# Performance work log

Hardware: AMD Instinct MI355X
Metric: run time of the kernel (lower is better)

## Reference

```python
import jax, jax.numpy as jnp
import numpy as np

NUM_USERS = 200000
NUM_ITEMS = 100000
N_NODES = NUM_USERS + NUM_ITEMS
NNZ = 4000000
LATENT_DIM = 64
N_LAYERS = 3


def setup_inputs() -> dict:
    key = jax.random.key(0)
    k1, k2, k3, k4, k5 = jax.random.split(key, 5)
    user_emb = jax.random.normal(k1, (NUM_USERS, LATENT_DIM), dtype=jnp.float32) * 0.1
    item_emb = jax.random.normal(k2, (NUM_ITEMS, LATENT_DIM), dtype=jnp.float32) * 0.1
    vals = jax.random.uniform(k3, (NNZ,), dtype=jnp.float32)
    rows = jax.random.randint(k4, (NNZ,), 0, N_NODES)
    cols = jax.random.randint(k5, (NNZ,), 0, N_NODES)
    return {"user_emb": user_emb, "item_emb": item_emb, "vals": vals,
            "rows": rows, "cols": cols}


def _spmm(vals, rows, cols, x):
    # y[r] += vals[e] * x[cols[e]]  -- COO SpMM, equivalent to torch.sparse.mm
    msgs = vals[:, None] * x[cols]          # [nnz, d]
    return jax.ops.segment_sum(msgs, rows, num_segments=N_NODES)


def reference(user_emb, item_emb, vals, rows, cols):
    # LightGCN.computer(), eval path: L = ones, no dropout, norm_emb=False
    all_emb = jnp.concatenate([user_emb, item_emb], axis=0)  # [N, d]
    emb = all_emb
    acc = all_emb
    for _ in range(N_LAYERS):
        emb = _spmm(vals, rows, cols, emb)
        acc = acc + emb
    light_out = acc / jnp.asarray(N_LAYERS + 1, dtype=acc.dtype)  # mean over layers
    users = light_out[:NUM_USERS]
    items = light_out[NUM_USERS:]
    return users, items
```

## Files before the change

kernel.cpp:

```cpp
#include <hip/hip_runtime.h>

#define NUM_USERS 200000
#define NUM_ITEMS 100000
#define N_NODES   300000
#define NNZ       4000000
#define DIM       64
#define N_ELEM   ((size_t)N_NODES * DIM)

static __device__ __forceinline__ float bf2f(unsigned short v) {
    return __uint_as_float(((unsigned int)v) << 16);
}
static __device__ __forceinline__ unsigned short f2bf(float f) {
    unsigned int u = __float_as_uint(f);
    u = (u + 0x7FFF + ((u >> 16) & 1)) >> 16;
    return (unsigned short)u;
}

__global__ void lgcn_hist(const int4* __restrict__ rows4, int* __restrict__ cnt) {
    int i = blockIdx.x * blockDim.x + threadIdx.x;
    if (i >= NNZ / 4) return;
    int4 r = rows4[i];
    atomicAdd(&cnt[r.x], 1);
    atomicAdd(&cnt[r.y], 1);
    atomicAdd(&cnt[r.z], 1);
    atomicAdd(&cnt[r.w], 1);
}

__global__ void lgcn_alloc(const int* __restrict__ cnt, int2* __restrict__ desc,
                           int* __restrict__ fill, int* __restrict__ cursor) {
    int r = blockIdx.x * blockDim.x + threadIdx.x;
    int lane = threadIdx.x & 63;
    int c = (r < N_NODES) ? cnt[r] : 0;
    int s = c;
    #pragma unroll
    for (int o = 1; o < 64; o <<= 1) {
        int t = __shfl_up(s, o);
        if (lane >= o) s += t;
    }
    int total = __shfl(s, 63);
    int wbase = 0;
    if (lane == 63) wbase = atomicAdd(cursor, total);
    wbase = __shfl(wbase, 63);
    if (r < N_NODES) {
        int b = wbase + (s - c);
        desc[r] = make_int2(b, c);
        fill[r] = b;
    }
}

__global__ void lgcn_scatter(const int* __restrict__ rows, const int* __restrict__ cols,
                             const float* __restrict__ vals, int* __restrict__ fill,
                             int2* __restrict__ sc) {
    int e = blockIdx.x * blockDim.x + threadIdx.x;
    if (e >= NNZ) return;
    int r = rows[e];
    int p = atomicAdd(&fill[r], 1);
    sc[p] = make_int2(cols[e], __float_as_int(vals[e]));
}

template<int MODE>
__global__ __launch_bounds__(256) void lgcn_spmm_csr(
    const int2* __restrict__ desc, const int2* __restrict__ sc,
    const float* __restrict__ user_emb, const float* __restrict__ item_emb,
    const unsigned short* __restrict__ cur, unsigned short* __restrict__ nxt,
    float* __restrict__ out)
{
    int row  = blockIdx.x * 4 + (threadIdx.x >> 6);
    int lane = threadIdx.x & 63;
    if (row >= N_NODES) return;
    int2 d = desc[row];
    int b = d.x, n = d.y;
    float acc0 = 0.f, acc1 = 0.f, acc2 = 0.f, acc3 = 0.f;

    for (int k0 = 0; k0 < n; k0 += 64) {
        int m = min(64, n - k0);
        int c = 0, vbits = 0;
        if (lane < m) {
            int2 cv = sc[b + k0 + lane];
            c = cv.x; vbits = cv.y;
        }
        int m8 = (m + 7) & ~7;
        for (int j = 0; j < m8; j += 8) {
            int   cc[8];
            float vv[8];
            #pragma unroll
            for (int t = 0; t < 8; ++t) {
                cc[t] = __shfl(c, j + t);
                vv[t] = __int_as_float(__shfl(vbits, j + t));
            }
            float x[8];
            #pragma unroll
            for (int t = 0; t < 8; ++t) {
                if constexpr (MODE == 0) {
                    x[t] = (cc[t] < NUM_USERS)
                         ? user_emb[(size_t)cc[t] * DIM + lane]
                         : item_emb[(size_t)(cc[t] - NUM_USERS) * DIM + lane];
                } else {
                    x[t] = bf2f(cur[(size_t)cc[t] * DIM + lane]);
                }
            }
            acc0 += vv[0] * x[0];
            acc1 += vv[1] * x[1];
            acc2 += vv[2] * x[2];
            acc3 += vv[3] * x[3];
            acc0 += vv[4] * x[4];
            acc1 += vv[5] * x[5];
            acc2 += vv[6] * x[6];
            acc3 += vv[7] * x[7];
        }
    }

    float acc = (acc0 + acc1) + (acc2 + acc3);
    size_t o = (size_t)row * DIM + lane;
    if constexpr (MODE == 0) {
        float own = (row < NUM_USERS)
                  ? user_emb[o]
                  : item_emb[(size_t)(row - NUM_USERS) * DIM + lane];
        nxt[o] = f2bf(acc);
        out[o] = 0.25f * (own + acc);
    } else if constexpr (MODE == 1) {
        nxt[o] = f2bf(acc);
        out[o] += 0.25f * acc;
    } else {
        out[o] += 0.25f * acc;
    }
}

extern "C" void kernel_launch(void* const* d_in, const int* in_sizes, int n_in,
                              void* d_out, int out_size, void* d_ws, size_t ws_size,
                              hipStream_t stream) {
    const float* user_emb = (const float*)d_in[0];
    const float* item_emb = (const float*)d_in[1];
    const float* vals     = (const float*)d_in[2];
    const int*   rows     = (const int*)d_in[3];
    const int*   cols     = (const int*)d_in[4];
    float* out = (float*)d_out;

    char* ws = (char*)d_ws;
    size_t off = 0;
    unsigned short* buf0 = (unsigned short*)(ws + off); off += N_ELEM * 2;
    unsigned short* buf1 = (unsigned short*)(ws + off); off += N_ELEM * 2;
    int2*  sc       = (int2*)(ws + off); off += (size_t)NNZ * 8;
    int*   row_cnt  = (int*) (ws + off); off += (size_t)N_NODES * 4;
    int*   cursor   = (int*) (ws + off); off += 256;
    int2*  row_desc = (int2*)(ws + off); off += (size_t)N_NODES * 8;
    int*   row_fill = (int*) (ws + off); off += (size_t)N_NODES * 4;

    const int BLK = 256;
    dim3 grid_edge((NNZ + BLK - 1) / BLK);
    dim3 grid_edge4((NNZ / 4 + BLK - 1) / BLK);
    dim3 grid_node((N_NODES + BLK - 1) / BLK);
    dim3 grid_spmm((N_NODES + 3) / 4);

    hipMemsetAsync(row_cnt, 0, (size_t)N_NODES * 4 + 256, stream);
    lgcn_hist<<<grid_edge4, BLK, 0, stream>>>((const int4*)rows, row_cnt);
    lgcn_alloc<<<grid_node, BLK, 0, stream>>>(row_cnt, row_desc, row_fill, cursor);
    lgcn_scatter<<<grid_edge, BLK, 0, stream>>>(rows, cols, vals, row_fill, sc);

    lgcn_spmm_csr<0><<<grid_spmm, BLK, 0, stream>>>(
        row_desc, sc, user_emb, item_emb, nullptr, buf0, out);
    lgcn_spmm_csr<1><<<grid_spmm, BLK, 0, stream>>>(
        row_desc, sc, nullptr, nullptr, buf0, buf1, out);
    lgcn_spmm_csr<2><<<grid_spmm, BLK, 0, stream>>>(
        row_desc, sc, nullptr, nullptr, buf1, nullptr, out);
}
```

Measured before the change: 952.5 us.

## Build CSR via two-level bucket sort and gather bf16 inputs in all layers

```diff
diff --git a/kernel.cpp b/kernel.cpp
--- a/kernel.cpp
+++ b/kernel.cpp
@@ -7,6 +7,10 @@
 #define DIM       64
 #define N_ELEM   ((size_t)N_NODES * DIM)
 
+#define BKT_SHIFT 6
+#define NBKT      ((N_NODES + 63) >> 6)
+#define PAD       32
+
 static __device__ __forceinline__ float bf2f(unsigned short v) {
     return __uint_as_float(((unsigned int)v) << 16);
 }
@@ -16,21 +20,33 @@
     return (unsigned short)u;
 }
 
-__global__ void lgcn_hist(const int4* __restrict__ rows4, int* __restrict__ cnt) {
+__global__ void lgcn_convert(const float4* __restrict__ user4,
+                             const float4* __restrict__ item4,
+                             ushort4* __restrict__ bufC) {
+    size_t i = (size_t)blockIdx.x * blockDim.x + threadIdx.x;
+    const size_t n4 = N_ELEM / 4, nu4 = (size_t)NUM_USERS * DIM / 4;
+    if (i >= n4) return;
+    float4 v = (i < nu4) ? user4[i] : item4[i - nu4];
+    ushort4 o;
+    o.x = f2bf(v.x); o.y = f2bf(v.y); o.z = f2bf(v.z); o.w = f2bf(v.w);
+    bufC[i] = o;
+}
+
+__global__ void lgcn_bhist(const int4* __restrict__ rows4, int* __restrict__ bcnt) {
     int i = blockIdx.x * blockDim.x + threadIdx.x;
     if (i >= NNZ / 4) return;
     int4 r = rows4[i];
-    atomicAdd(&cnt[r.x], 1);
-    atomicAdd(&cnt[r.y], 1);
-    atomicAdd(&cnt[r.z], 1);
-    atomicAdd(&cnt[r.w], 1);
-}
-
-__global__ void lgcn_alloc(const int* __restrict__ cnt, int2* __restrict__ desc,
-                           int* __restrict__ fill, int* __restrict__ cursor) {
-    int r = blockIdx.x * blockDim.x + threadIdx.x;
+    atomicAdd(&bcnt[(r.x >> BKT_SHIFT) * PAD], 1);
+    atomicAdd(&bcnt[(r.y >> BKT_SHIFT) * PAD], 1);
+    atomicAdd(&bcnt[(r.z >> BKT_SHIFT) * PAD], 1);
+    atomicAdd(&bcnt[(r.w >> BKT_SHIFT) * PAD], 1);
+}
+
+__global__ void lgcn_balloc(const int* __restrict__ bcnt, int* __restrict__ bbase,
+                            int* __restrict__ bfill, int* __restrict__ cursor) {
+    int b = blockIdx.x * blockDim.x + threadIdx.x;
     int lane = threadIdx.x & 63;
-    int c = (r < N_NODES) ? cnt[r] : 0;
+    int c = (b < NBKT) ? bcnt[b * PAD] : 0;
     int s = c;
     #pragma unroll
     for (int o = 1; o < 64; o <<= 1) {
@@ -41,28 +57,69 @@
     int wbase = 0;
     if (lane == 63) wbase = atomicAdd(cursor, total);
     wbase = __shfl(wbase, 63);
-    if (r < N_NODES) {
-        int b = wbase + (s - c);
-        desc[r] = make_int2(b, c);
-        fill[r] = b;
-    }
-}
-
-__global__ void lgcn_scatter(const int* __restrict__ rows, const int* __restrict__ cols,
-                             const float* __restrict__ vals, int* __restrict__ fill,
-                             int2* __restrict__ sc) {
+    if (b < NBKT) {
+        int base = wbase + (s - c);
+        bbase[b] = base;
+        bfill[b * PAD] = base;
+    }
+}
+
+__global__ void lgcn_append(const int* __restrict__ rows, const int* __restrict__ cols,
+                            const float* __restrict__ vals, int* __restrict__ bfill,
+                            int2* __restrict__ staging) {
     int e = blockIdx.x * blockDim.x + threadIdx.x;
     if (e >= NNZ) return;
     int r = rows[e];
-    int p = atomicAdd(&fill[r], 1);
-    sc[p] = make_int2(cols[e], __float_as_int(vals[e]));
+    int b = r >> BKT_SHIFT;
+    int p = atomicAdd(&bfill[b * PAD], 1);
+    staging[p] = make_int2(((r & 63) << 19) | cols[e], __float_as_int(vals[e]));
+}
+
+__global__ __launch_bounds__(256) void lgcn_bsort(
+    const int2* __restrict__ staging, const int* __restrict__ bbase,
+    const int* __restrict__ bcnt, int2* __restrict__ desc, int2* __restrict__ sc)
+{
+    __shared__ int cnt64[64], fill64[64];
+    int b   = blockIdx.x;
+    int tid = threadIdx.x;
+    if (tid < 64) cnt64[tid] = 0;
+    __syncthreads();
+    int base = bbase[b];
+    int n    = bcnt[b * PAD];
+
+    for (int i = tid; i < n; i += 256)
+        atomicAdd(&cnt64[staging[base + i].x >> 19], 1);
+    __syncthreads();
+
+    if (tid < 64) {
+        int c = cnt64[tid];
+        int s = c;
+        #pragma unroll
+        for (int o = 1; o < 64; o <<= 1) {
+            int t = __shfl_up(s, o);
+            if (tid >= o) s += t;
+        }
+        int off = s - c;
+        fill64[tid] = off;
+        int row = (b << BKT_SHIFT) + tid;
+        if (row < N_NODES) desc[row] = make_int2(base + off, c);
+    }
+    __syncthreads();
+
+    for (int i = tid; i < n; i += 256) {
+        int2 e = staging[base + i];
+        int lr = e.x >> 19;
+        int p = atomicAdd(&fill64[lr], 1);
+        sc[base + p] = make_int2(e.x & 0x7FFFF, e.y);
+    }
 }
 
 template<int MODE>
 __global__ __launch_bounds__(256) void lgcn_spmm_csr(
     const int2* __restrict__ desc, const int2* __restrict__ sc,
+    const unsigned short* __restrict__ cur, unsigned short* __restrict__ nxt,
     const float* __restrict__ user_emb, const float* __restrict__ item_emb,
-    const unsigned short* __restrict__ cur, unsigned short* __restrict__ nxt,
+    const unsigned short* __restrict__ e1buf, const unsigned short* __restrict__ e2buf,
     float* __restrict__ out)
 {
     int row  = blockIdx.x * 4 + (threadIdx.x >> 6);
@@ -90,15 +147,8 @@
             }
             float x[8];
             #pragma unroll
-            for (int t = 0; t < 8; ++t) {
-                if constexpr (MODE == 0) {
-                    x[t] = (cc[t] < NUM_USERS)
-                         ? user_emb[(size_t)cc[t] * DIM + lane]
-                         : item_emb[(size_t)(cc[t] - NUM_USERS) * DIM + lane];
-                } else {
-                    x[t] = bf2f(cur[(size_t)cc[t] * DIM + lane]);
-                }
-            }
+            for (int t = 0; t < 8; ++t)
+                x[t] = bf2f(cur[(size_t)cc[t] * DIM + lane]);
             acc0 += vv[0] * x[0];
             acc1 += vv[1] * x[1];
             acc2 += vv[2] * x[2];
@@ -112,17 +162,13 @@
 
     float acc = (acc0 + acc1) + (acc2 + acc3);
     size_t o = (size_t)row * DIM + lane;
-    if constexpr (MODE == 0) {
+    if constexpr (MODE == 1) {
+        nxt[o] = f2bf(acc);
+    } else {
         float own = (row < NUM_USERS)
                   ? user_emb[o]
                   : item_emb[(size_t)(row - NUM_USERS) * DIM + lane];
-        nxt[o] = f2bf(acc);
-        out[o] = 0.25f * (own + acc);
-    } else if constexpr (MODE == 1) {
-        nxt[o] = f2bf(acc);
-        out[o] += 0.25f * acc;
-    } else {
-        out[o] += 0.25f * acc;
+        out[o] = 0.25f * (own + bf2f(e1buf[o]) + bf2f(e2buf[o]) + acc);
     }
 }
 
@@ -138,29 +184,37 @@
 
     char* ws = (char*)d_ws;
     size_t off = 0;
+    unsigned short* bufC = (unsigned short*)(ws + off); off += N_ELEM * 2;
     unsigned short* buf0 = (unsigned short*)(ws + off); off += N_ELEM * 2;
     unsigned short* buf1 = (unsigned short*)(ws + off); off += N_ELEM * 2;
-    int2*  sc       = (int2*)(ws + off); off += (size_t)NNZ * 8;
-    int*   row_cnt  = (int*) (ws + off); off += (size_t)N_NODES * 4;
-    int*   cursor   = (int*) (ws + off); off += 256;
-    int2*  row_desc = (int2*)(ws + off); off += (size_t)N_NODES * 8;
-    int*   row_fill = (int*) (ws + off); off += (size_t)N_NODES * 4;
+    int2* staging = (int2*)(ws + off); off += (size_t)NNZ * 8;
+    int2* sc      = (int2*)(ws + off); off += (size_t)NNZ * 8;
+    int2* desc    = (int2*)(ws + off); off += (size_t)N_NODES * 8;
+    int*  bcnt    = (int*) (ws + off); off += (size_t)NBKT * PAD * 4;
+    int*  cursor  = (int*) (ws + off); off += 256;
+    int*  bbase   = (int*) (ws + off); off += (size_t)NBKT * 4;
+    int*  bfill   = (int*) (ws + off); off += (size_t)NBKT * PAD * 4;
 
     const int BLK = 256;
+    dim3 grid_conv((unsigned)((N_ELEM / 4 + BLK - 1) / BLK));
     dim3 grid_edge((NNZ + BLK - 1) / BLK);
     dim3 grid_edge4((NNZ / 4 + BLK - 1) / BLK);
-    dim3 grid_node((N_NODES + BLK - 1) / BLK);
+    dim3 grid_bkt((NBKT + BLK - 1) / BLK);
+    dim3 grid_sort(NBKT);
     dim3 grid_spmm((N_NODES + 3) / 4);
 
-    hipMemsetAsync(row_cnt, 0, (size_t)N_NODES * 4 + 256, stream);
-    lgcn_hist<<<grid_edge4, BLK, 0, stream>>>((const int4*)rows, row_cnt);
-    lgcn_alloc<<<grid_node, BLK, 0, stream>>>(row_cnt, row_desc, row_fill, cursor);
-    lgcn_scatter<<<grid_edge, BLK, 0, stream>>>(rows, cols, vals, row_fill, sc);
-
-    lgcn_spmm_csr<0><<<grid_spmm, BLK, 0, stream>>>(
-        row_desc, sc, user_emb, item_emb, nullptr, buf0, out);
+    hipMemsetAsync(bcnt, 0, (size_t)NBKT * PAD * 4 + 256, stream);
+    lgcn_convert<<<grid_conv, BLK, 0, stream>>>(
+        (const float4*)user_emb, (const float4*)item_emb, (ushort4*)bufC);
+    lgcn_bhist<<<grid_edge4, BLK, 0, stream>>>((const int4*)rows, bcnt);
+    lgcn_balloc<<<grid_bkt, BLK, 0, stream>>>(bcnt, bbase, bfill, cursor);
+    lgcn_append<<<grid_edge, BLK, 0, stream>>>(rows, cols, vals, bfill, staging);
+    lgcn_bsort<<<grid_sort, BLK, 0, stream>>>(staging, bbase, bcnt, desc, sc);
+
     lgcn_spmm_csr<1><<<grid_spmm, BLK, 0, stream>>>(
-        row_desc, sc, nullptr, nullptr, buf0, buf1, out);
+        desc, sc, bufC, buf0, nullptr, nullptr, nullptr, nullptr, nullptr);
+    lgcn_spmm_csr<1><<<grid_spmm, BLK, 0, stream>>>(
+        desc, sc, buf0, buf1, nullptr, nullptr, nullptr, nullptr, nullptr);
     lgcn_spmm_csr<2><<<grid_spmm, BLK, 0, stream>>>(
-        row_desc, sc, nullptr, nullptr, buf1, nullptr, out);
-}
+        desc, sc, buf1, nullptr, user_emb, item_emb, buf0, buf1, out);
+}
```

After: 957.1 us. No clear change (+0.5%).
